# Kernel tuning notes

Hardware: AMD Instinct MI355X
Metric: run time of the kernel (lower is better)

The kernel has to match this reference:

```python
import jax, jax.numpy as jnp
import numpy as np

BOUND = np.array([[-4.0, 4.0], [-4.0, 4.0], [-2.0, 2.0]], dtype=np.float32)
N_PTS = 1048576
PLANE_C = 3
PLANE_RES = [128, 256, 512, 1024]
N_LEVELS = 16
F_PER = 2
T = 2 ** 16  # hashmap size (log2_hashmap_size=16)
BASE_RES = 16
FINEST = int(float((BOUND[:, 1] - BOUND[:, 0]).max()) / 0.02)  # 400
_growth = np.exp(np.log(FINEST / BASE_RES) / (N_LEVELS - 1))
HASH_RES = np.floor(BASE_RES * _growth ** np.arange(N_LEVELS)).astype(np.float32)
PRIMES = jnp.array([1, 2654435761, 805459861], dtype=jnp.uint32)


def setup_inputs() -> dict:
    key = jax.random.key(0)
    ks = jax.random.split(key, 32)
    lo = jnp.asarray(BOUND[:, 0]); hi = jnp.asarray(BOUND[:, 1])
    inp = {}
    inp['p'] = jax.random.uniform(ks[0], (N_PTS, 3), dtype=jnp.float32) * (hi - lo) + lo
    i = 1
    for li, r in enumerate(PLANE_RES):
        for name in ('xy', 'xz', 'yz'):
            inp[f'plane_{name}_{li}'] = 0.1 * jax.random.normal(ks[i], (PLANE_C, r, r), dtype=jnp.float32)
            i += 1
    inp['hash_table'] = jax.random.uniform(ks[i], (N_LEVELS, T, F_PER), dtype=jnp.float32, minval=-1e-4, maxval=1e-4); i += 1

    def lin(k, fi, fo):
        s = 1.0 / np.sqrt(fi)
        k1, k2 = jax.random.split(k)
        return (jax.random.uniform(k1, (fi, fo), minval=-s, maxval=s, dtype=jnp.float32),
                jax.random.uniform(k2, (fo,), minval=-s, maxval=s, dtype=jnp.float32))

    c_in = 12 * PLANE_C + N_LEVELS * F_PER  # 68
    inp['W0'], inp['b0'] = lin(ks[i], c_in, 64); i += 1
    inp['W1'], inp['b1'] = lin(ks[i], 64, 64); i += 1
    inp['Wo'], inp['bo'] = lin(ks[i], 64, 33); i += 1  # 1 sdf + 32 geo_feat
    inp['Wc0'], inp['bc0'] = lin(ks[i], 12 * PLANE_C + 32, 64); i += 1
    inp['Wc1'], inp['bc1'] = lin(ks[i], 64, 32); i += 1
    inp['Wco'], inp['bco'] = lin(ks[i], 32, 3); i += 1
    return inp


def sample_plane(plane, u, v):
    """Bilinear grid_sample, align_corners=True, padding_mode='border'.
    plane: (C,H,W); u indexes W, v indexes H; u,v in [-1,1]. Returns (N,C)."""
    C, H, W = plane.shape
    x = jnp.clip((u + 1.0) * 0.5 * (W - 1), 0.0, W - 1)
    y = jnp.clip((v + 1.0) * 0.5 * (H - 1), 0.0, H - 1)
    x0 = jnp.floor(x); y0 = jnp.floor(y)
    wx = x - x0; wy = y - y0
    x0i = x0.astype(jnp.int32); y0i = y0.astype(jnp.int32)
    x1i = jnp.minimum(x0i + 1, W - 1); y1i = jnp.minimum(y0i + 1, H - 1)
    g = lambda yi, xi: plane[:, yi, xi]  # (C,N)
    out = (g(y0i, x0i) * ((1 - wy) * (1 - wx)) + g(y0i, x1i) * ((1 - wy) * wx)
           + g(y1i, x0i) * (wy * (1 - wx)) + g(y1i, x1i) * (wy * wx))
    return out.T


def hash_encode(p01, table):
    """Multi-res hash grid (instant-ngp style). p01: (N,3) in [0,1]; table: (L,T,F) -> (N, L*F)."""
    res = jnp.asarray(HASH_RES)  # (L,)

    def level(r, tab):
        x = p01 * r
        x0 = jnp.floor(x)
        w = x - x0
        xi = x0.astype(jnp.uint32)  # (N,3)
        feat = jnp.zeros((p01.shape[0], F_PER), dtype=table.dtype)
        for dz in (0, 1):
            for dy in (0, 1):
                for dx in (0, 1):
                    c = xi + jnp.array([dx, dy, dz], dtype=jnp.uint32)
                    h = c * PRIMES[None, :]
                    idx = ((h[:, 0] ^ h[:, 1] ^ h[:, 2]) % T).astype(jnp.int32)
                    wgt = ((w[:, 0] if dx else 1 - w[:, 0])
                           * (w[:, 1] if dy else 1 - w[:, 1])
                           * (w[:, 2] if dz else 1 - w[:, 2]))
                    feat = feat + tab[idx] * wgt[:, None]
        return feat  # (N,F)

    feats = jax.vmap(level, in_axes=(0, 0))(res, table)  # (L,N,F)
    return jnp.transpose(feats, (1, 0, 2)).reshape(p01.shape[0], N_LEVELS * F_PER)


def _forward(p, plane_xy_0, plane_xz_0, plane_yz_0, plane_xy_1, plane_xz_1, plane_yz_1,
             plane_xy_2, plane_xz_2, plane_yz_2, plane_xy_3, plane_xz_3, plane_yz_3,
             hash_table, W0, b0, W1, b1, Wo, bo, Wc0, bc0, Wc1, bc1, Wco, bco):
    bound = jnp.asarray(BOUND)
    p_nor = (p - bound[:, 0]) / (bound[:, 1] - bound[:, 0]) * 2.0 - 1.0  # normalize_3d_coordinate
    u, v, w = p_nor[:, 0], p_nor[:, 1], p_nor[:, 2]
    levels = [(plane_xy_0, plane_xz_0, plane_yz_0), (plane_xy_1, plane_xz_1, plane_yz_1),
              (plane_xy_2, plane_xz_2, plane_yz_2), (plane_xy_3, plane_xz_3, plane_yz_3)]
    feats = []
    for pxy, pxz, pyz in levels:
        feats += [sample_plane(pxy, u, v), sample_plane(pxz, u, w), sample_plane(pyz, v, w)]
    plane_feat = jnp.concatenate(feats, axis=-1)  # (N, 36)
    hfeat = hash_encode((p_nor + 1.0) * 0.5, hash_table)  # (N, 32)
    # SDF branch
    h = jnp.concatenate([plane_feat, hfeat], axis=-1)  # (N, 68)
    h = jax.nn.relu(h @ W0 + b0)
    h = jax.nn.relu(h @ W1 + b1)
    sf = jnp.tanh(h @ Wo + bo)
    sdf, geo_feat = sf[:, :1], sf[:, 1:]
    # RGB branch
    c = jnp.concatenate([geo_feat, plane_feat], axis=-1)  # (N, 68)
    c = jax.nn.relu(c @ Wc0 + bc0)
    c = jax.nn.relu(c @ Wc1 + bc1)
    rgb = jax.nn.sigmoid(c @ Wco + bco)
    return jnp.concatenate([rgb, sdf], axis=-1)  # (N, 4)


def reference(p, plane_xy_0, plane_xz_0, plane_yz_0, plane_xy_1, plane_xz_1, plane_yz_1,
              plane_xy_2, plane_xz_2, plane_yz_2, plane_xy_3, plane_xz_3, plane_yz_3,
              hash_table, W0, b0, W1, b1, Wo, bo, Wc0, bc0, Wc1, bc1, Wco, bco):
    return _forward(p, plane_xy_0, plane_xz_0, plane_yz_0, plane_xy_1, plane_xz_1, plane_yz_1,
                    plane_xy_2, plane_xz_2, plane_yz_2, plane_xy_3, plane_xz_3, plane_yz_3,
                    hash_table, W0, b0, W1, b1, Wo, bo, Wc0, bc0, Wc1, bc1, Wco, bco)
```

## Files before the change

### kernel.cpp

```cpp
#include <hip/hip_runtime.h>

#define NPTS 1048576
#define NBKT 262144

typedef short bhalf8 __attribute__((ext_vector_type(8)));
typedef _Float16 halfv8 __attribute__((ext_vector_type(8)));
typedef _Float16 halfv2 __attribute__((ext_vector_type(2)));
typedef float floatx4 __attribute__((ext_vector_type(4)));

#define WSZ 24320
#define FROWS 21
#define MLP_THREADS 1024
#define MLP_WAVES 16

#define PB_PLANES 16320
#define PB_HASH 4096
#define PB_HIST 4096

__device__ const float HRg[16] = {16.f, 19.f, 24.f, 30.f, 37.f, 46.f, 57.f, 71.f,
                                  89.f, 110.f, 136.f, 169.f, 210.f, 260.f, 322.f, 400.f};


__device__ __forceinline__ float my_tanh(float x) {
  float e = __expf(2.f * x);
  return 1.f - 2.f * __builtin_amdgcn_rcpf(e + 1.f);
}

__device__ __forceinline__ float my_sigmoid(float x) {
  return __builtin_amdgcn_rcpf(1.f + __expf(-x));
}

__device__ __forceinline__ unsigned short f2h(float v) {
  _Float16 h = (_Float16)v;
  unsigned short u;
  __builtin_memcpy(&u, &h, 2);
  return u;
}

__device__ __forceinline__ float h2f(unsigned short u) {
  _Float16 h;
  __builtin_memcpy(&h, &u, 2);
  return (float)h;
}

// ... 19 lines not shown

__device__ __forceinline__ unsigned hash_level(const unsigned* __restrict__ ht, int lv,
                                               float q0, float q1, float q2) {
  const float r = HRg[lv];
  float x0 = q0 * r, x1 = q1 * r, x2 = q2 * r;
  float f0 = floorf(x0), f1 = floorf(x1), f2 = floorf(x2);
  float w0 = x0 - f0, w1 = x1 - f1, w2 = x2 - f2;
  unsigned i0 = (unsigned)(int)f0, i1 = (unsigned)(int)f1, i2 = (unsigned)(int)f2;
  const unsigned* __restrict__ hb = ht + ((unsigned)lv << 16);
  unsigned tv[8];
#pragma unroll
  for (int dz = 0; dz < 2; ++dz)
#pragma unroll
    for (int dy = 0; dy < 2; ++dy)
#pragma unroll
      for (int dx = 0; dx < 2; ++dx) {
        unsigned h = (i0 + dx) ^ ((i1 + dy) * 2654435761u) ^ ((i2 + dz) * 805459861u);
        tv[dz * 4 + dy * 2 + dx] = hb[h & 65535u];
      }
  halfv2 acc2 = {(_Float16)0.f, (_Float16)0.f};
#pragma unroll
  for (int c = 0; c < 8; ++c) {
    const int dx = c & 1, dy = (c >> 1) & 1, dz = c >> 2;
    float wgt = (dx ? w0 : 1.f - w0) * (dy ? w1 : 1.f - w1) * (dz ? w2 : 1.f - w2);
    halfv2 th;
    __builtin_memcpy(&th, &tv[c], 4);
    _Float16 wh = (_Float16)wgt;
    halfv2 w2v = {wh, wh};
    acc2 = th * w2v + acc2;
  }
  unsigned res;
  __builtin_memcpy(&res, &acc2, 4);
  return res;
}


struct PrepParams {
  const float* psrc[12];
  ushort4* pdst[12];
  const float* hash;
  unsigned* hashb;
  const float* p;
  unsigned* hist;
};

__global__ __launch_bounds__(256) void prep_kernel(PrepParams P) {
  const int b = blockIdx.x;
  if (b < PB_PLANES) {
    const int CUM[13] = {0, 16384, 32768, 49152, 114688, 180224, 245760,
                         507904, 770048, 1032192, 2080768, 3129344, 4177920};
    const int RESL[12] = {128, 128, 128, 256, 256, 256, 512, 512, 512, 1024, 1024, 1024};
    const int s = b << 8;
    int pi = 0;
#pragma unroll
    for (int i = 1; i < 12; ++i)
      if (s >= CUM[i]) pi = i;
    const int li = s + threadIdx.x - CUM[pi];
    const int R = RESL[pi];
    const int n = R * R;
    const float* __restrict__ src = P.psrc[pi];
    ushort4 t;
    t.x = f2h(src[li]);
    t.y = f2h(src[n + li]);
    t.z = f2h(src[2 * n + li]);
    t.w = 0;
    P.pdst[pi][li] = t;
  } else if (b < PB_PLANES + PB_HASH) {
    const int i = ((b - PB_PLANES) << 8) + threadIdx.x;
    float2 v = *(const float2*)(P.hash + (size_t)i * 2);
    P.hashb[i] = (unsigned)f2h(v.x) | ((unsigned)f2h(v.y) << 16);
  } else {
    const int i = ((b - PB_PLANES - PB_HASH) << 8) + threadIdx.x;
    const float* pp = P.p + (size_t)i * 3;
    unsigned k = morton_key(pp[0], pp[1], pp[2]);
    atomicAdd(&P.hist[k], 1u);
  }
}


__global__ __launch_bounds__(256) void scan1_kernel(const unsigned* __restrict__ hist,
                                                    unsigned* __restrict__ partial) {
  __shared__ unsigned s[256];
  const int b = blockIdx.x, t = threadIdx.x;
  uint4 v = ((const uint4*)(hist + b * 1024))[t];
  s[t] = v.x + v.y + v.z + v.w;
  __syncthreads();
  for (int d = 128; d > 0; d >>= 1) {
    if (t < d) s[t] += s[t + d];
    __syncthreads();
  }
  if (t == 0) partial[b] = s[0];
}

__global__ __launch_bounds__(256) void scan2_kernel(const unsigned* __restrict__ partial,
                                                    unsigned* __restrict__ base) {
  __shared__ unsigned s[256];
  const int t = threadIdx.x;
  s[t] = partial[t];
  __syncthreads();
  for (int d = 1; d < 256; d <<= 1) {
    unsigned v = (t >= d) ? s[t - d] : 0u;
    __syncthreads();
    s[t] += v;
    __syncthreads();
  }
  base[t] = (t == 0) ? 0u : s[t - 1];
}

__global__ __launch_bounds__(256) void scan3_kernel(const unsigned* __restrict__ hist,
                                                    const unsigned* __restrict__ base,
                                                    unsigned* __restrict__ cursor) {
  __shared__ unsigned s[256];
  const int b = blockIdx.x, t = threadIdx.x;
  uint4 v = ((const uint4*)(hist + b * 1024))[t];
  unsigned sum = v.x + v.y + v.z + v.w;
  s[t] = sum;
  __syncthreads();
  for (int d = 1; d < 256; d <<= 1) {
    unsigned x = (t >= d) ? s[t - d] : 0u;
    __syncthreads();
    s[t] += x;
    __syncthreads();
  }
  unsigned off = base[b] + s[t] - sum;
  uint4 c;
  c.x = off;
  c.y = off + v.x;
  c.z = off + v.x + v.y;
  c.w = off + v.x + v.y + v.z;
  ((uint4*)(cursor + b * 1024))[t] = c;
}

__global__ __launch_bounds__(256) void scatter_kernel(const float* __restrict__ p,
                                                      unsigned* __restrict__ cursor,
                                                      unsigned* __restrict__ perm) {
  int i = blockIdx.x * 256 + threadIdx.x;
  const float* pp = p + (size_t)i * 3;
  unsigned k = morton_key(pp[0], pp[1], pp[2]);
  unsigned slot = atomicAdd(&cursor[k], 1u);
  perm[slot] = (unsigned)i;
}


__global__ __launch_bounds__(256) void repack_plane(const float* __restrict__ src,
                                                    ushort4* __restrict__ dst, int R) {
  int i = blockIdx.x * 256 + threadIdx.x;
  int n = R * R;
  if (i >= n) return;
  ushort4 t;
  t.x = f2h(src[i]);
  t.y = f2h(src[n + i]);
  t.z = f2h(src[2 * n + i]);
  t.w = 0;
  dst[i] = t;
}


__device__ __forceinline__ void sample3i(const uint2* __restrict__ pl,
                                         float a, float b, int R, float* f) {
  const float Rm1 = (float)(R - 1);
  float x = fminf(fmaxf((a + 1.f) * 0.5f * Rm1, 0.f), Rm1);
  float y = fminf(fmaxf((b + 1.f) * 0.5f * Rm1, 0.f), Rm1);
  float x0f = floorf(x), y0f = floorf(y);
  float wx = x - x0f, wy = y - y0f;
  int x0 = (int)x0f, y0 = (int)y0f;
  int x1 = min(x0 + 1, R - 1), y1 = min(y0 + 1, R - 1);
  float w00 = (1.f - wy) * (1.f - wx);
  float w01 = (1.f - wy) * wx;
  float w10 = wy * (1.f - wx);
  float w11 = wy * wx;
  uint2 t00 = pl[y0 * R + x0];
  uint2 t01 = pl[y0 * R + x1];
  uint2 t10 = pl[y1 * R + x0];
  uint2 t11 = pl[y1 * R + x1];
#pragma unroll
  for (int c = 0; c < 3; ++c) {
    f[c] = texch(t00, c) * w00 + texch(t01, c) * w01 +
           texch(t10, c) * w10 + texch(t11, c) * w11;
  }
}

__device__ __forceinline__ void sample3f(const float* __restrict__ pl,
                                         float a, float b, int R, float* f) {
  const float Rm1 = (float)(R - 1);
  float x = fminf(fmaxf((a + 1.f) * 0.5f * Rm1, 0.f), Rm1);
  float y = fminf(fmaxf((b + 1.f) * 0.5f * Rm1, 0.f), Rm1);
  float x0f = floorf(x), y0f = floorf(y);
  float wx = x - x0f, wy = y - y0f;
  int x0 = (int)x0f, y0 = (int)y0f;
  int x1 = min(x0 + 1, R - 1), y1 = min(y0 + 1, R - 1);
  float w00 = (1.f - wy) * (1.f - wx);
  float w01 = (1.f - wy) * wx;
  float w10 = wy * (1.f - wx);
  float w11 = wy * wx;
  int i00 = y0 * R + x0, i01 = y0 * R + x1;
  int i10 = y1 * R + x0, i11 = y1 * R + x1;
  const int R2 = R * R;
#pragma unroll
  for (int c = 0; c < 3; ++c) {
    const float* base = pl + c * R2;
    f[c] = base[i00] * w00 + base[i01] * w01 + base[i10] * w10 + base[i11] * w11;
  }
}


struct FeatParams {
  const float* p;
  const uint2* pli[12];
  const unsigned* perm;
  unsigned* fbuf;
};

template <bool SORT>
__global__ __launch_bounds__(256) void feat_kernel(FeatParams P) {
  int bid = blockIdx.x;
  if (SORT) bid = (bid & 7) * (NPTS / 256 / 8) + (bid >> 3);
  const int tid = bid * 256 + threadIdx.x;
  const int pid = SORT ? (int)P.perm[tid] : tid;

  const float* __restrict__ pp = P.p + (size_t)pid * 3;
  const float px = pp[0], py = pp[1], pz = pp[2];

  const float u = (px + 4.f) * 0.25f - 1.f;
  const float v = (py + 4.f) * 0.25f - 1.f;
  const float w = (pz + 2.f) * 0.5f - 1.f;

  float pf[36];
  {
    const int RES[4] = {128, 256, 512, 1024};
#pragma unroll
    for (int li = 0; li < 4; ++li) {
      sample3i(P.pli[li * 3 + 0], u, v, RES[li], &pf[li * 9 + 0]);
      sample3i(P.pli[li * 3 + 1], u, w, RES[li], &pf[li * 9 + 3]);
      sample3i(P.pli[li * 3 + 2], v, w, RES[li], &pf[li * 9 + 6]);
    }
  }
  unsigned* __restrict__ F = P.fbuf;
#pragma unroll
  for (int kk = 0; kk < 18; ++kk) {
    unsigned pk = (unsigned)f2h(pf[2 * kk]) | ((unsigned)f2h(pf[2 * kk + 1]) << 16);
    F[(size_t)kk * NPTS + tid] = pk;
  }
  F[(size_t)18 * NPTS + tid] = __float_as_uint((px + 4.f) * 0.125f);
  F[(size_t)19 * NPTS + tid] = __float_as_uint((py + 4.f) * 0.125f);
  F[(size_t)20 * NPTS + tid] = __float_as_uint((pz + 2.f) * 0.25f);
}


struct MlpWParams {
  const unsigned* fbuf;
  const unsigned* perm;
  const unsigned* hashb;
  const float* W0; const float* b0;
  const float* W1; const float* b1;
  const float* Wo; const float* bo;
  const float* Wc0; const float* bc0;
  const float* Wc1; const float* bc1;
  const float* Wco; const float* bco;
  float* out;
};

__device__ __forceinline__ void stage_w(const float* __restrict__ src, int K, int Nsrc,
                                        int STR, int NPAD, int OFF, short* Wlds, int tid) {
  const int total = NPAD * STR;
  for (int idx = tid; idx < total; idx += MLP_THREADS) {
    int c = idx / STR;
    int k = idx - c * STR;
    float val = (k < K && c < Nsrc) ? src[k * Nsrc + c] : 0.f;
    Wlds[OFF + idx] = (short)f2h(val);
  }
}

__device__ __forceinline__ void stage_b(const float* __restrict__ src, int Nsrc, int NPAD,
                                        int BOFF, float* Blds, int tid) {
  for (int j = tid; j < NPAD; j += MLP_THREADS) Blds[BOFF + j] = (j < Nsrc) ? src[j] : 0.f;
}

__device__ __forceinline__ halfv8 as_h8(bhalf8 s) {
  halfv8 h;
  __builtin_memcpy(&h, &s, 16);
  return h;
}

__device__ __forceinline__ halfv8 ldA(const unsigned* __restrict__ fbuf, int pt,
                                      int kkBase, int kkLim) {
  bhalf8 r;
#pragma unroll
  for (int j = 0; j < 4; ++j) {
    const int kk = kkBase + j;
    unsigned d = 0u;
    if (kk < kkLim) d = fbuf[(size_t)kk * NPTS + pt];
    r[2 * j] = (short)(d & 0xffffu);
    r[2 * j + 1] = (short)(d >> 16);
  }
  return as_h8(r);
}

__device__ __forceinline__ halfv8 frag4(unsigned d0, unsigned d1, unsigned d2, unsigned d3) {
  bhalf8 r;
  r[0] = (short)(d0 & 0xffffu); r[1] = (short)(d0 >> 16);
  r[2] = (short)(d1 & 0xffffu); r[3] = (short)(d1 >> 16);
  r[4] = (short)(d2 & 0xffffu); r[5] = (short)(d2 >> 16);
  r[6] = (short)(d3 & 0xffffu); r[7] = (short)(d3 >> 16);
  return as_h8(r);
}

__device__ __forceinline__ halfv8 ldS(const short* scr, int rowl, int grp, int s) {
  return *(const halfv8*)&scr[rowl * 72 + 32 * s + 8 * grp];
}

template <int NT, int KS, int OFF, int STR>
__device__ __forceinline__ void mlayer(const halfv8 (&af)[KS], floatx4 (&acc)[NT],
                                       const short* Wlds, int rowl, int grp) {
#pragma unroll
  for (int n = 0; n < NT; ++n) {
    floatx4 a{};
#pragma unroll
    for (int s = 0; s < KS; ++s) {
      const int wo = OFF + (16 * n + rowl) * STR + 32 * s + 8 * grp;
      const halfv8 wA = *(const halfv8*)&Wlds[wo];
      a = __builtin_amdgcn_mfma_f32_16x16x32_f16(wA, af[s], a, 0, 0, 0);
    }
    acc[n] = a;
  }
}

template <int NT>
__device__ __forceinline__ void relu_wr(const floatx4 (&acc)[NT], const float* Blds,
                                        int boff, short* scr, int rowl, int grp) {
#pragma unroll
  for (int n = 0; n < NT; ++n) {
    const int cbase = 16 * n + 4 * grp;
    short4 v4;
    float v0 = fmaxf(acc[n][0] + Blds[boff + cbase + 0], 0.f);
    float v1 = fmaxf(acc[n][1] + Blds[boff + cbase + 1], 0.f);
    float v2 = fmaxf(acc[n][2] + Blds[boff + cbase + 2], 0.f);
    float v3 = fmaxf(acc[n][3] + Blds[boff + cbase + 3], 0.f);
    v4.x = (short)f2h(v0);
    v4.y = (short)f2h(v1);
    v4.z = (short)f2h(v2);
    v4.w = (short)f2h(v3);
    *(short4*)&scr[rowl * 72 + cbase] = v4;
  }
}

__device__ __forceinline__ void tanh_wr(const floatx4 (&acc)[3], const float* Blds,
                                        short* scr, float* ost, int rowl, int grp) {
#pragma unroll
  for (int n = 0; n < 3; ++n) {
#pragma unroll
    for (int r = 0; r < 4; ++r) {
      const int c = 16 * n + 4 * grp + r;
      float v = my_tanh(acc[n][r] + Blds[128 + c]);
      if (c == 0) ost[rowl * 4 + 3] = v;
      if (c >= 1 && c <= 32) scr[rowl * 72 + c - 1] = (short)f2h(v);
    }
  }
}

template <bool SORT>
__global__ __launch_bounds__(MLP_THREADS) void mlp_mfma(MlpWParams P) {
  __shared__ short Wlds[WSZ];
  __shared__ float Blds[288];
  __shared__ short Scr[MLP_WAVES * 16 * 72];
  __shared__ float Ost[MLP_WAVES][16][4];

  const int tid = threadIdx.x;

  stage_w(P.W0,  68, 64, 104, 64,     0, Wlds, tid);
  stage_w(P.W1,  64, 64,  72, 64,  6656, Wlds, tid);
  stage_w(P.Wo,  64, 33,  72, 48, 11264, Wlds, tid);
  stage_w(P.Wc0, 68, 64, 104, 64, 14720, Wlds, tid);
  stage_w(P.Wc1, 64, 32,  72, 32, 21376, Wlds, tid);
  stage_w(P.Wco, 32,  3,  40, 16, 23680, Wlds, tid);
  stage_b(P.b0,  64, 64,   0, Blds, tid);
  stage_b(P.b1,  64, 64,  64, Blds, tid);
  stage_b(P.bo,  33, 48, 128, Blds, tid);
  stage_b(P.bc0, 64, 64, 176, Blds, tid);
  stage_b(P.bc1, 32, 32, 240, Blds, tid);
  stage_b(P.bco,  3, 16, 272, Blds, tid);
  __syncthreads();

  const int wave = tid >> 6, lane = tid & 63;
  const int rowl = lane & 15, grp = lane >> 4;
  short* scr0 = &Scr[wave * 16 * 72];
  float* ost0 = &Ost[wave][0][0];

  const int lv0 = (grp == 0) ? 0 : (4 * grp - 2);

  for (int t = 0; t < 8; ++t) {
    const int wbase = ((blockIdx.x * 8 + t) * MLP_WAVES + wave) * 16;
    const int ptA = wbase + rowl;

    halfv8 af0A;
    unsigned pA16, pA17;

    {
      const unsigned* __restrict__ F = P.fbuf;
      float qA0 = __uint_as_float(F[(size_t)18 * NPTS + ptA]);
      float qA1 = __uint_as_float(F[(size_t)19 * NPTS + ptA]);
      float qA2 = __uint_as_float(F[(size_t)20 * NPTS + ptA]);

      unsigned hA0, hA1, hA2, hA3;
      {
        const int l0 = lv0, l1 = lv0 + 1;
        const int l2 = (grp == 0) ? 14 : (lv0 + 2);
        const int l3 = (grp == 0) ? 15 : (lv0 + 3);
        hA0 = hash_level(P.hashb, l0, qA0, qA1, qA2);
        hA1 = hash_level(P.hashb, l1, qA0, qA1, qA2);
        hA2 = hash_level(P.hashb, l2, qA0, qA1, qA2);
        hA3 = hash_level(P.hashb, l3, qA0, qA1, qA2);
      }

      pA16 = F[(size_t)16 * NPTS + ptA];
      pA17 = F[(size_t)17 * NPTS + ptA];

      halfv8 s1A = (grp == 0) ? frag4(pA16, pA17, hA0, hA1) : frag4(hA0, hA1, hA2, hA3);
      halfv8 s2A = (grp == 0) ? frag4(hA2, hA3, 0u, 0u) : frag4(0u, 0u, 0u, 0u);

      af0A = ldA(P.fbuf, ptA, 4 * grp, 18);
      halfv8 afA[3] = {af0A, s1A, s2A};
      floatx4 accA[4];
      mlayer<4, 3, 0, 104>(afA, accA, Wlds, rowl, grp);
      relu_wr<4>(accA, Blds, 0, scr0, rowl, grp);
    }
    {
      halfv8 afA[2] = {ldS(scr0, rowl, grp, 0), ldS(scr0, rowl, grp, 1)};
      floatx4 accA[4];
      mlayer<4, 2, 6656, 72>(afA, accA, Wlds, rowl, grp);
      relu_wr<4>(accA, Blds, 64, scr0, rowl, grp);
    }
    {
      halfv8 afA[2] = {ldS(scr0, rowl, grp, 0), ldS(scr0, rowl, grp, 1)};
      floatx4 accA[3];
      mlayer<3, 2, 11264, 72>(afA, accA, Wlds, rowl, grp);
      tanh_wr(accA, Blds, scr0, ost0, rowl, grp);
    }
    {
      halfv8 s2 = (grp == 0) ? frag4(pA16, pA17, 0u, 0u) : frag4(0u, 0u, 0u, 0u);
      halfv8 afA[3] = {ldS(scr0, rowl, grp, 0), af0A, s2};
      floatx4 accA[4];
      mlayer<4, 3, 14720, 104>(afA, accA, Wlds, rowl, grp);
      relu_wr<4>(accA, Blds, 176, scr0, rowl, grp);
    }
    {
      halfv8 afA[2] = {ldS(scr0, rowl, grp, 0), ldS(scr0, rowl, grp, 1)};
      floatx4 accA[2];
      mlayer<2, 2, 21376, 72>(afA, accA, Wlds, rowl, grp);
      relu_wr<2>(accA, Blds, 240, scr0, rowl, grp);
    }
    {
      halfv8 afA[1] = {ldS(scr0, rowl, grp, 0)};
      floatx4 accA[1];
      mlayer<1, 1, 23680, 40>(afA, accA, Wlds, rowl, grp);
#pragma unroll
      for (int r = 0; r < 4; ++r) {
        const int c = 4 * grp + r;
        if (c < 3) {
          float vA = my_sigmoid(accA[0][r] + Blds[272 + c]);
          ost0[rowl * 4 + c] = vA;
        }
      }
    }

    if (lane < 16) {
      float4 o = *(float4*)&Ost[wave][lane][0];
      int dst = SORT ? (int)P.perm[wbase + lane] : (wbase + lane);
      ((float4*)P.out)[dst] = o;
    }
  }
}


struct DecParams {
  const float* p;
  const float* pl[12];
  const uint2* pli[12];
  const float* hash;
  const float* W0; const float* b0;
  const float* W1; const float* b1;
  const float* Wo; const float* bo;
  const float* Wc0; const float* bc0;
  const float* Wc1; const float* bc1;
  const float* Wco; const float* bco;
  float* out;
};

template <bool ILV>
__global__ __launch_bounds__(256) void dec_kernel(DecParams P) {
  const int tid = blockIdx.x * 256 + threadIdx.x;

  const float* __restrict__ pp = P.p + (size_t)tid * 3;
  const float px = pp[0], py = pp[1], pz = pp[2];

  const float u = (px + 4.f) * 0.25f - 1.f;
  const float v = (py + 4.f) * 0.25f - 1.f;
  const float w = (pz + 2.f) * 0.5f - 1.f;

  float feat[68];
  {
    const int RES[4] = {128, 256, 512, 1024};
// ... 105 lines not shown
  float c1[32];
#pragma unroll
  for (int j = 0; j < 32; ++j) c1[j] = P.bc1[j];
#pragma unroll
  for (int i = 0; i < 64; ++i) {
    const float a = hid[i];
    const float* wr = P.Wc1 + i * 32;
#pragma unroll
    for (int j = 0; j < 32; ++j) c1[j] = fmaf(a, wr[j], c1[j]);
  }

  float r0 = P.bco[0], r1 = P.bco[1], r2 = P.bco[2];
#pragma unroll
  for (int i = 0; i < 32; ++i) {
    const float a = fmaxf(c1[i], 0.f);
    r0 = fmaf(a, P.Wco[i * 3 + 0], r0);
    r1 = fmaf(a, P.Wco[i * 3 + 1], r1);
    r2 = fmaf(a, P.Wco[i * 3 + 2], r2);
  }

  float4 o;
  o.x = my_sigmoid(r0);
  o.y = my_sigmoid(r1);
  o.z = my_sigmoid(r2);
  o.w = sdf;
  ((float4*)P.out)[tid] = o;
}


extern "C" void kernel_launch(void* const* d_in, const int* in_sizes, int n_in,
                              void* d_out, int out_size, void* d_ws, size_t ws_size,
                              hipStream_t stream) {
  const int RES[4] = {128, 256, 512, 1024};
  const size_t planes_bytes = (size_t)3 * (128 * 128 + 256 * 256 + 512 * 512 + 1024 * 1024) * 8;
  const size_t hash_bytes = (size_t)16 * 65536 * 4;
  const size_t feat_bytes = (size_t)FROWS * NPTS * 4;
  const size_t perm_bytes = (size_t)NPTS * 4;
  const size_t hist_bytes = (size_t)NBKT * 4;
  const size_t need_full = planes_bytes + hash_bytes + feat_bytes + 64;
  const size_t need_sort = need_full + perm_bytes + 2 * hist_bytes + 4096;
  const size_t need_mid = planes_bytes + 64;

  char* wsp = (char*)d_ws;
  const float* p = (const float*)d_in[0];

  if (ws_size >= need_sort) {
    size_t off = 0;
    PrepParams PP;
    PP.p = p;
    PP.hash = (const float*)d_in[13];
    const uint2* pli[12];
    for (int i = 0; i < 12; ++i) {
      int R = RES[i / 3];
      PP.psrc[i] = (const float*)d_in[1 + i];
      PP.pdst[i] = (ushort4*)(wsp + off);
      pli[i] = (const uint2*)(wsp + off);
      off += (size_t)R * R * 8;
    }
    unsigned* hashb = (unsigned*)(wsp + off);
    PP.hashb = hashb;
    off += hash_bytes;
    unsigned* fbuf = (unsigned*)(wsp + off);
    off += feat_bytes;
    unsigned* perm = (unsigned*)(wsp + off);
    off += perm_bytes;
    unsigned* hist = (unsigned*)(wsp + off);
    off += hist_bytes;
    unsigned* cursor = (unsigned*)(wsp + off);
    off += hist_bytes;
    unsigned* partial = (unsigned*)(wsp + off);
    off += 1024;
    unsigned* base = (unsigned*)(wsp + off);
    off += 1024;
    PP.hist = hist;

    hipMemsetAsync(hist, 0, hist_bytes, stream);
    prep_kernel<<<PB_PLANES + PB_HASH + PB_HIST, 256, 0, stream>>>(PP);
    scan1_kernel<<<256, 256, 0, stream>>>(hist, partial);
    scan2_kernel<<<1, 256, 0, stream>>>(partial, base);
    scan3_kernel<<<256, 256, 0, stream>>>(hist, base, cursor);
    scatter_kernel<<<NPTS / 256, 256, 0, stream>>>(p, cursor, perm);

    FeatParams FP;
    FP.p = p;
    for (int i = 0; i < 12; ++i) FP.pli[i] = pli[i];
    FP.perm = perm;
    FP.fbuf = fbuf;
    feat_kernel<true><<<NPTS / 256, 256, 0, stream>>>(FP);

    MlpWParams MP;
    MP.fbuf = fbuf;
    MP.perm = perm;
    MP.hashb = hashb;
    MP.W0 = (const float*)d_in[14]; MP.b0 = (const float*)d_in[15];
    MP.W1 = (const float*)d_in[16]; MP.b1 = (const float*)d_in[17];
    MP.Wo = (const float*)d_in[18]; MP.bo = (const float*)d_in[19];
    MP.Wc0 = (const float*)d_in[20]; MP.bc0 = (const float*)d_in[21];
    MP.Wc1 = (const float*)d_in[22]; MP.bc1 = (const float*)d_in[23];
    MP.Wco = (const float*)d_in[24]; MP.bco = (const float*)d_in[25];
    MP.out = (float*)d_out;
    mlp_mfma<true><<<512, MLP_THREADS, 0, stream>>>(MP);
    return;
  }

  if (ws_size >= need_full) {
    size_t off = 0;
    PrepParams PP;
    PP.p = p;
    PP.hash = (const float*)d_in[13];
    const uint2* pli[12];
    for (int i = 0; i < 12; ++i) {
      int R = RES[i / 3];
      PP.psrc[i] = (const float*)d_in[1 + i];
      PP.pdst[i] = (ushort4*)(wsp + off);
      pli[i] = (const uint2*)(wsp + off);
      off += (size_t)R * R * 8;
    }
    unsigned* hashb = (unsigned*)(wsp + off);
    PP.hashb = hashb;
    off += hash_bytes;
    unsigned* fbuf = (unsigned*)(wsp + off);
    PP.hist = nullptr;

    prep_kernel<<<PB_PLANES + PB_HASH, 256, 0, stream>>>(PP);

    FeatParams FP;
    FP.p = p;
    for (int i = 0; i < 12; ++i) FP.pli[i] = pli[i];
    FP.perm = nullptr;
    FP.fbuf = fbuf;
    feat_kernel<false><<<NPTS / 256, 256, 0, stream>>>(FP);

    MlpWParams MP;
    MP.fbuf = fbuf;
    MP.perm = nullptr;
    MP.hashb = hashb;
    MP.W0 = (const float*)d_in[14]; MP.b0 = (const float*)d_in[15];
    MP.W1 = (const float*)d_in[16]; MP.b1 = (const float*)d_in[17];
    MP.Wo = (const float*)d_in[18]; MP.bo = (const float*)d_in[19];
    MP.Wc0 = (const float*)d_in[20]; MP.bc0 = (const float*)d_in[21];
    MP.Wc1 = (const float*)d_in[22]; MP.bc1 = (const float*)d_in[23];
    MP.Wco = (const float*)d_in[24]; MP.bco = (const float*)d_in[25];
    MP.out = (float*)d_out;
    mlp_mfma<false><<<512, MLP_THREADS, 0, stream>>>(MP);
    return;
  }

  DecParams P;
  P.p = p;
  for (int i = 0; i < 12; ++i) P.pl[i] = (const float*)d_in[1 + i];
  P.hash = (const float*)d_in[13];
  P.W0  = (const float*)d_in[14]; P.b0  = (const float*)d_in[15];
  P.W1  = (const float*)d_in[16]; P.b1  = (const float*)d_in[17];
  P.Wo  = (const float*)d_in[18]; P.bo  = (const float*)d_in[19];
  P.Wc0 = (const float*)d_in[20]; P.bc0 = (const float*)d_in[21];
  P.Wc1 = (const float*)d_in[22]; P.bc1 = (const float*)d_in[23];
  P.Wco = (const float*)d_in[24]; P.bco = (const float*)d_in[25];
  P.out = (float*)d_out;

  if (ws_size >= need_mid) {
    size_t off = 0;
    for (int i = 0; i < 12; ++i) {
      int R = RES[i / 3];
      int n = R * R;
      P.pli[i] = (const uint2*)(wsp + off);
      repack_plane<<<(n + 255) / 256, 256, 0, stream>>>(
          (const float*)d_in[1 + i], (ushort4*)(wsp + off), R);
      off += (size_t)n * 8;
    }
    dec_kernel<true><<<NPTS / 256, 256, 0, stream>>>(P);
  } else {
    for (int i = 0; i < 12; ++i) P.pli[i] = nullptr;
    dec_kernel<false><<<NPTS / 256, 256, 0, stream>>>(P);
  }
}
```

Before: 388.8 us.

## Fuse plane sampling into MLP kernel and scatter sorted coords directly

Drops the separate feature kernel and its 21-row intermediate buffer. Plane bilinear sampling now runs inside the MLP kernel on packed fp16 planes, with each lane group sampling planes that match its MFMA K-slice, and the W0/Wc0 staging is remapped to the new padded 4-channel layout. The scatter kernel writes sorted normalized coordinates plus the original index as a float4, which replaces the perm indirection. This removes a large global write/read round trip, at the cost of more gather latency and register pressure inside the MLP kernel, and the non-sort fallback path is removed.

```diff
diff --git a/kernel.cpp b/kernel.cpp
--- a/kernel.cpp
+++ b/kernel.cpp
@@ -9,7 +9,6 @@
 typedef float floatx4 __attribute__((ext_vector_type(4)));
 
 #define WSZ 24320
-#define FROWS 21
 #define MLP_THREADS 1024
 #define MLP_WAVES 16
 
@@ -95,6 +94,43 @@
   unsigned res;
   __builtin_memcpy(&res, &acc2, 4);
   return res;
+}
+
+__device__ __forceinline__ uint2 sampleP(const uint2* __restrict__ planes, int s,
+                                         float u, float v, float w) {
+  const int level = s / 3;
+  const int m = s - level * 3;
+  const float a = (m == 2) ? v : u;
+  const float b = (m == 0) ? v : w;
+  const int R = 128 << level;
+  const unsigned base = 16384u * ((1u << (2 * level)) - 1u) + (unsigned)m * (unsigned)(R * R);
+  const float Rm1 = (float)(R - 1);
+  float x = fminf(fmaxf((a + 1.f) * 0.5f * Rm1, 0.f), Rm1);
+  float y = fminf(fmaxf((b + 1.f) * 0.5f * Rm1, 0.f), Rm1);
+  float x0f = floorf(x), y0f = floorf(y);
+  float wx = x - x0f, wy = y - y0f;
+  int x0 = (int)x0f, y0 = (int)y0f;
+  int x1 = min(x0 + 1, R - 1), y1 = min(y0 + 1, R - 1);
+  uint2 t00 = planes[base + y0 * R + x0];
+  uint2 t01 = planes[base + y0 * R + x1];
+  uint2 t10 = planes[base + y1 * R + x0];
+  uint2 t11 = planes[base + y1 * R + x1];
+  _Float16 h00 = (_Float16)((1.f - wy) * (1.f - wx));
+  _Float16 h01 = (_Float16)((1.f - wy) * wx);
+  _Float16 h10 = (_Float16)(wy * (1.f - wx));
+  _Float16 h11 = (_Float16)(wy * wx);
+  halfv2 w00 = {h00, h00}, w01 = {h01, h01}, w10 = {h10, h10}, w11 = {h11, h11};
+  halfv2 l00, l01, l10, l11, u00, u01, u10, u11;
+  __builtin_memcpy(&l00, &t00.x, 4); __builtin_memcpy(&u00, &t00.y, 4);
+  __builtin_memcpy(&l01, &t01.x, 4); __builtin_memcpy(&u01, &t01.y, 4);
+  __builtin_memcpy(&l10, &t10.x, 4); __builtin_memcpy(&u10, &t10.y, 4);
+  __builtin_memcpy(&l11, &t11.x, 4); __builtin_memcpy(&u11, &t11.y, 4);
+  halfv2 alo = l00 * w00 + l01 * w01 + l10 * w10 + l11 * w11;
+  halfv2 ahi = u00 * w00 + u01 * w01 + u10 * w10 + u11 * w11;
+  uint2 r;
+  __builtin_memcpy(&r.x, &alo, 4);
+  __builtin_memcpy(&r.y, &ahi, 4);
+  return r;
 }
 
 
@@ -196,12 +232,18 @@
 
 __global__ __launch_bounds__(256) void scatter_kernel(const float* __restrict__ p,
                                                       unsigned* __restrict__ cursor,
-                                                      unsigned* __restrict__ perm) {
+                                                      float4* __restrict__ qs) {
   int i = blockIdx.x * 256 + threadIdx.x;
   const float* pp = p + (size_t)i * 3;
-  unsigned k = morton_key(pp[0], pp[1], pp[2]);
+  const float px = pp[0], py = pp[1], pz = pp[2];
+  unsigned k = morton_key(px, py, pz);
   unsigned slot = atomicAdd(&cursor[k], 1u);
-  perm[slot] = (unsigned)i;
+  float4 q;
+  q.x = (px + 4.f) * 0.125f;
+  q.y = (py + 4.f) * 0.125f;
+  q.z = (pz + 2.f) * 0.25f;
+  q.w = __uint_as_float((unsigned)i);
+  qs[slot] = q;
 }
 
 
@@ -267,53 +309,10 @@
 }
 
 
-struct FeatParams {
-  const float* p;
-  const uint2* pli[12];
-  const unsigned* perm;
-  unsigned* fbuf;
-};
-
-template <bool SORT>
-__global__ __launch_bounds__(256) void feat_kernel(FeatParams P) {
-  int bid = blockIdx.x;
-  if (SORT) bid = (bid & 7) * (NPTS / 256 / 8) + (bid >> 3);
-  const int tid = bid * 256 + threadIdx.x;
-  const int pid = SORT ? (int)P.perm[tid] : tid;
-
-  const float* __restrict__ pp = P.p + (size_t)pid * 3;
-  const float px = pp[0], py = pp[1], pz = pp[2];
-
-  const float u = (px + 4.f) * 0.25f - 1.f;
-  const float v = (py + 4.f) * 0.25f - 1.f;
-  const float w = (pz + 2.f) * 0.5f - 1.f;
-
-  float pf[36];
-  {
-    const int RES[4] = {128, 256, 512, 1024};
-#pragma unroll
-    for (int li = 0; li < 4; ++li) {
-      sample3i(P.pli[li * 3 + 0], u, v, RES[li], &pf[li * 9 + 0]);
-      sample3i(P.pli[li * 3 + 1], u, w, RES[li], &pf[li * 9 + 3]);
-      sample3i(P.pli[li * 3 + 2], v, w, RES[li], &pf[li * 9 + 6]);
-    }
-  }
-  unsigned* __restrict__ F = P.fbuf;
-#pragma unroll
-  for (int kk = 0; kk < 18; ++kk) {
-    unsigned pk = (unsigned)f2h(pf[2 * kk]) | ((unsigned)f2h(pf[2 * kk + 1]) << 16);
-    F[(size_t)kk * NPTS + tid] = pk;
-  }
-  F[(size_t)18 * NPTS + tid] = __float_as_uint((px + 4.f) * 0.125f);
-  F[(size_t)19 * NPTS + tid] = __float_as_uint((py + 4.f) * 0.125f);
-  F[(size_t)20 * NPTS + tid] = __float_as_uint((pz + 2.f) * 0.25f);
-}
-
-
 struct MlpWParams {
-  const unsigned* fbuf;
-  const unsigned* perm;
+  const uint2* planes;
   const unsigned* hashb;
+  const float4* qs;
   const float* W0; const float* b0;
   const float* W1; const float* b1;
   const float* Wo; const float* bo;
@@ -323,13 +322,32 @@
   float* out;
 };
 
+template <int MODE>
 __device__ __forceinline__ void stage_w(const float* __restrict__ src, int K, int Nsrc,
                                         int STR, int NPAD, int OFF, short* Wlds, int tid) {
   const int total = NPAD * STR;
   for (int idx = tid; idx < total; idx += MLP_THREADS) {
     int c = idx / STR;
-    int k = idx - c * STR;
-    float val = (k < K && c < Nsrc) ? src[k * Nsrc + c] : 0.f;
+    int kp = idx - c * STR;
+    int sk = -1;
+    if (MODE == 0) {
+      if (kp < 48) {
+        int s = kp >> 2, ch = kp & 3;
+        if (ch < 3) sk = s * 3 + ch;
+      } else if (kp < 80) {
+        sk = 36 + (kp - 48);
+      }
+    } else if (MODE == 1) {
+      if (kp < 32) {
+        sk = kp;
+      } else if (kp < 80) {
+        int s = (kp - 32) >> 2, ch = (kp - 32) & 3;
+        if (ch < 3) sk = 32 + s * 3 + ch;
+      }
+    } else {
+      if (kp < K) sk = kp;
+    }
+    float val = (sk >= 0 && c < Nsrc) ? src[sk * Nsrc + c] : 0.f;
     Wlds[OFF + idx] = (short)f2h(val);
   }
 }
@@ -343,20 +361,6 @@
   halfv8 h;
   __builtin_memcpy(&h, &s, 16);
   return h;
-}
-
-__device__ __forceinline__ halfv8 ldA(const unsigned* __restrict__ fbuf, int pt,
-                                      int kkBase, int kkLim) {
-  bhalf8 r;
-#pragma unroll
-  for (int j = 0; j < 4; ++j) {
-    const int kk = kkBase + j;
-    unsigned d = 0u;
-    if (kk < kkLim) d = fbuf[(size_t)kk * NPTS + pt];
-    r[2 * j] = (short)(d & 0xffffu);
-    r[2 * j + 1] = (short)(d >> 16);
-  }
-  return as_h8(r);
 }
 
 __device__ __forceinline__ halfv8 frag4(unsigned d0, unsigned d1, unsigned d2, unsigned d3) {
@@ -421,8 +425,7 @@
   }
 }
 
-template <bool SORT>
-__global__ __launch_bounds__(MLP_THREADS) void mlp_mfma(MlpWParams P) {
+__global__ __launch_bounds__(MLP_THREADS) void mlp_fused(MlpWParams P) {
   __shared__ short Wlds[WSZ];
   __shared__ float Blds[288];
   __shared__ short Scr[MLP_WAVES * 16 * 72];
@@ -430,12 +433,12 @@
 
   const int tid = threadIdx.x;
 
-  stage_w(P.W0,  68, 64, 104, 64,     0, Wlds, tid);
-  stage_w(P.W1,  64, 64,  72, 64,  6656, Wlds, tid);
-  stage_w(P.Wo,  64, 33,  72, 48, 11264, Wlds, tid);
-  stage_w(P.Wc0, 68, 64, 104, 64, 14720, Wlds, tid);
-  stage_w(P.Wc1, 64, 32,  72, 32, 21376, Wlds, tid);
-  stage_w(P.Wco, 32,  3,  40, 16, 23680, Wlds, tid);
+  stage_w<0>(P.W0,  96, 64, 104, 64,     0, Wlds, tid);
+  stage_w<2>(P.W1,  64, 64,  72, 64,  6656, Wlds, tid);
+  stage_w<2>(P.Wo,  64, 33,  72, 48, 11264, Wlds, tid);
+  stage_w<1>(P.Wc0, 96, 64, 104, 64, 14720, Wlds, tid);
+  stage_w<2>(P.Wc1, 64, 32,  72, 32, 21376, Wlds, tid);
+  stage_w<2>(P.Wco, 32,  3,  40, 16, 23680, Wlds, tid);
   stage_b(P.b0,  64, 64,   0, Blds, tid);
   stage_b(P.b1,  64, 64,  64, Blds, tid);
   stage_b(P.bo,  33, 48, 128, Blds, tid);
@@ -449,40 +452,40 @@
   short* scr0 = &Scr[wave * 16 * 72];
   float* ost0 = &Ost[wave][0][0];
 
-  const int lv0 = (grp == 0) ? 0 : (4 * grp - 2);
+  int bid = blockIdx.x;
+  bid = (bid & 7) * 64 + (bid >> 3);
 
   for (int t = 0; t < 8; ++t) {
-    const int wbase = ((blockIdx.x * 8 + t) * MLP_WAVES + wave) * 16;
-    const int ptA = wbase + rowl;
-
-    halfv8 af0A;
-    unsigned pA16, pA17;
+    const int wbase = ((bid * 8 + t) * MLP_WAVES + wave) * 16;
+    const int pt = wbase + rowl;
+
+    float4 q4 = P.qs[pt];
+    const float q0 = q4.x, q1 = q4.y, q2 = q4.z;
+    const unsigned pid = __float_as_uint(q4.w);
+    const float u = 2.f * q0 - 1.f;
+    const float v = 2.f * q1 - 1.f;
+    const float w = 2.f * q2 - 1.f;
+
+    uint2 sA = sampleP(P.planes, 2 * grp, u, v, w);
+    uint2 sB = sampleP(P.planes, 2 * grp + 1, u, v, w);
+    uint2 sC = {0u, 0u}, sD = {0u, 0u};
+    if (grp < 2) {
+      sC = sampleP(P.planes, 8 + 2 * grp, u, v, w);
+      sD = sampleP(P.planes, 9 + 2 * grp, u, v, w);
+    }
+    const int lbase = (grp < 2) ? (8 + 4 * grp) : (4 * grp - 8);
+    unsigned h0 = hash_level(P.hashb, lbase + 0, q0, q1, q2);
+    unsigned h1 = hash_level(P.hashb, lbase + 1, q0, q1, q2);
+    unsigned h2 = hash_level(P.hashb, lbase + 2, q0, q1, q2);
+    unsigned h3 = hash_level(P.hashb, lbase + 3, q0, q1, q2);
+
+    halfv8 af0 = frag4(sA.x, sA.y, sB.x, sB.y);
+    halfv8 af1 = (grp < 2) ? frag4(sC.x, sC.y, sD.x, sD.y) : frag4(h0, h1, h2, h3);
+    halfv8 af2 = (grp < 2) ? frag4(h0, h1, h2, h3) : frag4(0u, 0u, 0u, 0u);
+    halfv8 zf = frag4(0u, 0u, 0u, 0u);
 
     {
-      const unsigned* __restrict__ F = P.fbuf;
-      float qA0 = __uint_as_float(F[(size_t)18 * NPTS + ptA]);
-      float qA1 = __uint_as_float(F[(size_t)19 * NPTS + ptA]);
-      float qA2 = __uint_as_float(F[(size_t)20 * NPTS + ptA]);
-
-      unsigned hA0, hA1, hA2, hA3;
-      {
-        const int l0 = lv0, l1 = lv0 + 1;
-        const int l2 = (grp == 0) ? 14 : (lv0 + 2);
-        const int l3 = (grp == 0) ? 15 : (lv0 + 3);
-        hA0 = hash_level(P.hashb, l0, qA0, qA1, qA2);
-        hA1 = hash_level(P.hashb, l1, qA0, qA1, qA2);
-        hA2 = hash_level(P.hashb, l2, qA0, qA1, qA2);
-        hA3 = hash_level(P.hashb, l3, qA0, qA1, qA2);
-      }
-
-      pA16 = F[(size_t)16 * NPTS + ptA];
-      pA17 = F[(size_t)17 * NPTS + ptA];
-
-      halfv8 s1A = (grp == 0) ? frag4(pA16, pA17, hA0, hA1) : frag4(hA0, hA1, hA2, hA3);
-      halfv8 s2A = (grp == 0) ? frag4(hA2, hA3, 0u, 0u) : frag4(0u, 0u, 0u, 0u);
-
-      af0A = ldA(P.fbuf, ptA, 4 * grp, 18);
-      halfv8 afA[3] = {af0A, s1A, s2A};
+      halfv8 afA[3] = {af0, af1, af2};
       floatx4 accA[4];
       mlayer<4, 3, 0, 104>(afA, accA, Wlds, rowl, grp);
       relu_wr<4>(accA, Blds, 0, scr0, rowl, grp);
@@ -500,8 +503,7 @@
       tanh_wr(accA, Blds, scr0, ost0, rowl, grp);
     }
     {
-      halfv8 s2 = (grp == 0) ? frag4(pA16, pA17, 0u, 0u) : frag4(0u, 0u, 0u, 0u);
-      halfv8 afA[3] = {ldS(scr0, rowl, grp, 0), af0A, s2};
+      halfv8 afA[3] = {ldS(scr0, rowl, grp, 0), af0, (grp < 2) ? af1 : zf};
       floatx4 accA[4];
       mlayer<4, 3, 14720, 104>(afA, accA, Wlds, rowl, grp);
       relu_wr<4>(accA, Blds, 176, scr0, rowl, grp);
@@ -528,8 +530,7 @@
 
     if (lane < 16) {
       float4 o = *(float4*)&Ost[wave][lane][0];
-      int dst = SORT ? (int)P.perm[wbase + lane] : (wbase + lane);
-      ((float4*)P.out)[dst] = o;
+      ((float4*)P.out)[pid] = o;
     }
   }
 }
@@ -701,38 +702,33 @@
                               void* d_out, int out_size, void* d_ws, size_t ws_size,
                               hipStream_t stream) {
   const int RES[4] = {128, 256, 512, 1024};
-  const size_t planes_bytes = (size_t)3 * (128 * 128 + 256 * 256 + 512 * 512 + 1024 * 1024) * 8;
+  const size_t planes_bytes = (size_t)4177920 * 8;
   const size_t hash_bytes = (size_t)16 * 65536 * 4;
-  const size_t feat_bytes = (size_t)FROWS * NPTS * 4;
-  const size_t perm_bytes = (size_t)NPTS * 4;
+  const size_t qs_bytes = (size_t)NPTS * 16;
   const size_t hist_bytes = (size_t)NBKT * 4;
-  const size_t need_full = planes_bytes + hash_bytes + feat_bytes + 64;
-  const size_t need_sort = need_full + perm_bytes + 2 * hist_bytes + 4096;
+  const size_t need_fused = planes_bytes + hash_bytes + qs_bytes + 2 * hist_bytes + 4096;
   const size_t need_mid = planes_bytes + 64;
 
   char* wsp = (char*)d_ws;
   const float* p = (const float*)d_in[0];
 
-  if (ws_size >= need_sort) {
+  if (ws_size >= need_fused) {
     size_t off = 0;
     PrepParams PP;
     PP.p = p;
     PP.hash = (const float*)d_in[13];
-    const uint2* pli[12];
+    const uint2* planes = (const uint2*)wsp;
     for (int i = 0; i < 12; ++i) {
       int R = RES[i / 3];
       PP.psrc[i] = (const float*)d_in[1 + i];
       PP.pdst[i] = (ushort4*)(wsp + off);
-      pli[i] = (const uint2*)(wsp + off);
       off += (size_t)R * R * 8;
     }
     unsigned* hashb = (unsigned*)(wsp + off);
     PP.hashb = hashb;
     off += hash_bytes;
-    unsigned* fbuf = (unsigned*)(wsp + off);
-    off += feat_bytes;
-    unsigned* perm = (unsigned*)(wsp + off);
-    off += perm_bytes;
+    float4* qs = (float4*)(wsp + off);
+    off += qs_bytes;
     unsigned* hist = (unsigned*)(wsp + off);
     off += hist_bytes;
     unsigned* cursor = (unsigned*)(wsp + off);
@@ -748,19 +744,12 @@
     scan1_kernel<<<256, 256, 0, stream>>>(hist, partial);
     scan2_kernel<<<1, 256, 0, stream>>>(partial, base);
     scan3_kernel<<<256, 256, 0, stream>>>(hist, base, cursor);
-    scatter_kernel<<<NPTS / 256, 256, 0, stream>>>(p, cursor, perm);
-
-    FeatParams FP;
-    FP.p = p;
-    for (int i = 0; i < 12; ++i) FP.pli[i] = pli[i];
-    FP.perm = perm;
-    FP.fbuf = fbuf;
-    feat_kernel<true><<<NPTS / 256, 256, 0, stream>>>(FP);
+    scatter_kernel<<<NPTS / 256, 256, 0, stream>>>(p, cursor, qs);
 
     MlpWParams MP;
-    MP.fbuf = fbuf;
-    MP.perm = perm;
+    MP.planes = planes;
     MP.hashb = hashb;
+    MP.qs = qs;
     MP.W0 = (const float*)d_in[14]; MP.b0 = (const float*)d_in[15];
     MP.W1 = (const float*)d_in[16]; MP.b1 = (const float*)d_in[17];
     MP.Wo = (const float*)d_in[18]; MP.bo = (const float*)d_in[19];
@@ -768,50 +757,7 @@
     MP.Wc1 = (const float*)d_in[22]; MP.bc1 = (const float*)d_in[23];
     MP.Wco = (const float*)d_in[24]; MP.bco = (const float*)d_in[25];
     MP.out = (float*)d_out;
-    mlp_mfma<true><<<512, MLP_THREADS, 0, stream>>>(MP);
-    return;
-  }
-
-  if (ws_size >= need_full) {
-    size_t off = 0;
-    PrepParams PP;
-    PP.p = p;
-    PP.hash = (const float*)d_in[13];
-    const uint2* pli[12];
-    for (int i = 0; i < 12; ++i) {
-      int R = RES[i / 3];
-      PP.psrc[i] = (const float*)d_in[1 + i];
-      PP.pdst[i] = (ushort4*)(wsp + off);
-      pli[i] = (const uint2*)(wsp + off);
-      off += (size_t)R * R * 8;
-    }
-    unsigned* hashb = (unsigned*)(wsp + off);
-    PP.hashb = hashb;
-    off += hash_bytes;
-    unsigned* fbuf = (unsigned*)(wsp + off);
-    PP.hist = nullptr;
-
-    prep_kernel<<<PB_PLANES + PB_HASH, 256, 0, stream>>>(PP);
-
-    FeatParams FP;
-    FP.p = p;
-    for (int i = 0; i < 12; ++i) FP.pli[i] = pli[i];
-    FP.perm = nullptr;
-    FP.fbuf = fbuf;
-    feat_kernel<false><<<NPTS / 256, 256, 0, stream>>>(FP);
-
-    MlpWParams MP;
-    MP.fbuf = fbuf;
-    MP.perm = nullptr;
-    MP.hashb = hashb;
-    MP.W0 = (const float*)d_in[14]; MP.b0 = (const float*)d_in[15];
-    MP.W1 = (const float*)d_in[16]; MP.b1 = (const float*)d_in[17];
-    MP.Wo = (const float*)d_in[18]; MP.bo = (const float*)d_in[19];
-    MP.Wc0 = (const float*)d_in[20]; MP.bc0 = (const float*)d_in[21];
-    MP.Wc1 = (const float*)d_in[22]; MP.bc1 = (const float*)d_in[23];
-    MP.Wco = (const float*)d_in[24]; MP.bco = (const float*)d_in[25];
-    MP.out = (float*)d_out;
-    mlp_mfma<false><<<512, MLP_THREADS, 0, stream>>>(MP);
+    mlp_fused<<<512, MLP_THREADS, 0, stream>>>(MP);
     return;
   }
 
```

Result: slower. 418.8 us (+7.7%).

## Scatter normalized coordinates directly into sorted order and merge scan kernels

Applied to the files above, without the earlier changes.

The scatter kernel now writes each point's normalized coordinates and original index as a float4 into sorted slots, replacing the permutation array. The feature kernel therefore reads contiguous float4s instead of gathering through perm into p. The original index is carried as an extra feature row so the MLP can write outputs directly. The second and third scan kernels are merged into one, removing a launch and the base buffer. The MLP block order is also swizzled, and the unsorted fallback path is removed, so the kernel now needs the larger sort workspace.

```diff
diff --git a/kernel.cpp b/kernel.cpp
--- a/kernel.cpp
+++ b/kernel.cpp
@@ -9,7 +9,7 @@
 typedef float floatx4 __attribute__((ext_vector_type(4)));
 
 #define WSZ 24320
-#define FROWS 21
+#define FROWS 22
 #define MLP_THREADS 1024
 #define MLP_WAVES 16
 
@@ -155,37 +155,33 @@
   if (t == 0) partial[b] = s[0];
 }
 
-__global__ __launch_bounds__(256) void scan2_kernel(const unsigned* __restrict__ partial,
-                                                    unsigned* __restrict__ base) {
-  __shared__ unsigned s[256];
-  const int t = threadIdx.x;
-  s[t] = partial[t];
+__global__ __launch_bounds__(256) void scan23_kernel(const unsigned* __restrict__ hist,
+                                                     const unsigned* __restrict__ partial,
+                                                     unsigned* __restrict__ cursor) {
+  __shared__ unsigned sp[256];
+  __shared__ unsigned s2[256];
+  const int b = blockIdx.x, t = threadIdx.x;
+  sp[t] = partial[t];
   __syncthreads();
   for (int d = 1; d < 256; d <<= 1) {
-    unsigned v = (t >= d) ? s[t - d] : 0u;
+    unsigned v = (t >= d) ? sp[t - d] : 0u;
     __syncthreads();
-    s[t] += v;
+    sp[t] += v;
     __syncthreads();
   }
-  base[t] = (t == 0) ? 0u : s[t - 1];
-}
-
-__global__ __launch_bounds__(256) void scan3_kernel(const unsigned* __restrict__ hist,
-                                                    const unsigned* __restrict__ base,
-                                                    unsigned* __restrict__ cursor) {
-  __shared__ unsigned s[256];
-  const int b = blockIdx.x, t = threadIdx.x;
+  const unsigned base = (b == 0) ? 0u : sp[b - 1];
+
   uint4 v = ((const uint4*)(hist + b * 1024))[t];
   unsigned sum = v.x + v.y + v.z + v.w;
-  s[t] = sum;
+  s2[t] = sum;
   __syncthreads();
   for (int d = 1; d < 256; d <<= 1) {
-    unsigned x = (t >= d) ? s[t - d] : 0u;
+    unsigned x = (t >= d) ? s2[t - d] : 0u;
     __syncthreads();
-    s[t] += x;
+    s2[t] += x;
     __syncthreads();
   }
-  unsigned off = base[b] + s[t] - sum;
+  unsigned off = base + s2[t] - sum;
   uint4 c;
   c.x = off;
   c.y = off + v.x;
@@ -196,12 +192,18 @@
 
 __global__ __launch_bounds__(256) void scatter_kernel(const float* __restrict__ p,
                                                       unsigned* __restrict__ cursor,
-                                                      unsigned* __restrict__ perm) {
+                                                      float4* __restrict__ qs) {
   int i = blockIdx.x * 256 + threadIdx.x;
   const float* pp = p + (size_t)i * 3;
-  unsigned k = morton_key(pp[0], pp[1], pp[2]);
+  const float px = pp[0], py = pp[1], pz = pp[2];
+  unsigned k = morton_key(px, py, pz);
   unsigned slot = atomicAdd(&cursor[k], 1u);
-  perm[slot] = (unsigned)i;
+  float4 q;
+  q.x = (px + 4.f) * 0.125f;
+  q.y = (py + 4.f) * 0.125f;
+  q.z = (pz + 2.f) * 0.25f;
+  q.w = __uint_as_float((unsigned)i);
+  qs[slot] = q;
 }
 
 
@@ -268,25 +270,20 @@
 
 
 struct FeatParams {
-  const float* p;
+  const float4* qs;
   const uint2* pli[12];
-  const unsigned* perm;
   unsigned* fbuf;
 };
 
-template <bool SORT>
 __global__ __launch_bounds__(256) void feat_kernel(FeatParams P) {
   int bid = blockIdx.x;
-  if (SORT) bid = (bid & 7) * (NPTS / 256 / 8) + (bid >> 3);
+  bid = (bid & 7) * (NPTS / 256 / 8) + (bid >> 3);
   const int tid = bid * 256 + threadIdx.x;
-  const int pid = SORT ? (int)P.perm[tid] : tid;
-
-  const float* __restrict__ pp = P.p + (size_t)pid * 3;
-  const float px = pp[0], py = pp[1], pz = pp[2];
-
-  const float u = (px + 4.f) * 0.25f - 1.f;
-  const float v = (py + 4.f) * 0.25f - 1.f;
-  const float w = (pz + 2.f) * 0.5f - 1.f;
+
+  float4 q4 = P.qs[tid];
+  const float u = 2.f * q4.x - 1.f;
+  const float v = 2.f * q4.y - 1.f;
+  const float w = 2.f * q4.z - 1.f;
 
   float pf[36];
   {
@@ -304,15 +301,15 @@
     unsigned pk = (unsigned)f2h(pf[2 * kk]) | ((unsigned)f2h(pf[2 * kk + 1]) << 16);
     F[(size_t)kk * NPTS + tid] = pk;
   }
-  F[(size_t)18 * NPTS + tid] = __float_as_uint((px + 4.f) * 0.125f);
-  F[(size_t)19 * NPTS + tid] = __float_as_uint((py + 4.f) * 0.125f);
-  F[(size_t)20 * NPTS + tid] = __float_as_uint((pz + 2.f) * 0.25f);
+  F[(size_t)18 * NPTS + tid] = __float_as_uint(q4.x);
+  F[(size_t)19 * NPTS + tid] = __float_as_uint(q4.y);
+  F[(size_t)20 * NPTS + tid] = __float_as_uint(q4.z);
+  F[(size_t)21 * NPTS + tid] = __float_as_uint(q4.w);
 }
 
 
 struct MlpWParams {
   const unsigned* fbuf;
-  const unsigned* perm;
   const unsigned* hashb;
   const float* W0; const float* b0;
   const float* W1; const float* b1;
@@ -421,7 +418,6 @@
   }
 }
 
-template <bool SORT>
 __global__ __launch_bounds__(MLP_THREADS) void mlp_mfma(MlpWParams P) {
   __shared__ short Wlds[WSZ];
   __shared__ float Blds[288];
@@ -451,18 +447,23 @@
 
   const int lv0 = (grp == 0) ? 0 : (4 * grp - 2);
 
+  int bid = blockIdx.x;
+  bid = (bid & 7) * 64 + (bid >> 3);
+
   for (int t = 0; t < 8; ++t) {
-    const int wbase = ((blockIdx.x * 8 + t) * MLP_WAVES + wave) * 16;
+    const int wbase = ((bid * 8 + t) * MLP_WAVES + wave) * 16;
     const int ptA = wbase + rowl;
 
     halfv8 af0A;
     unsigned pA16, pA17;
+    unsigned pid;
 
     {
       const unsigned* __restrict__ F = P.fbuf;
       float qA0 = __uint_as_float(F[(size_t)18 * NPTS + ptA]);
       float qA1 = __uint_as_float(F[(size_t)19 * NPTS + ptA]);
       float qA2 = __uint_as_float(F[(size_t)20 * NPTS + ptA]);
+      pid = F[(size_t)21 * NPTS + ptA];
 
       unsigned hA0, hA1, hA2, hA3;
       {
@@ -528,8 +529,7 @@
 
     if (lane < 16) {
       float4 o = *(float4*)&Ost[wave][lane][0];
-      int dst = SORT ? (int)P.perm[wbase + lane] : (wbase + lane);
-      ((float4*)P.out)[dst] = o;
+      ((float4*)P.out)[pid] = o;
     }
   }
 }
@@ -701,13 +701,13 @@
                               void* d_out, int out_size, void* d_ws, size_t ws_size,
                               hipStream_t stream) {
   const int RES[4] = {128, 256, 512, 1024};
-  const size_t planes_bytes = (size_t)3 * (128 * 128 + 256 * 256 + 512 * 512 + 1024 * 1024) * 8;
+  const size_t planes_bytes = (size_t)4177920 * 8;
   const size_t hash_bytes = (size_t)16 * 65536 * 4;
   const size_t feat_bytes = (size_t)FROWS * NPTS * 4;
-  const size_t perm_bytes = (size_t)NPTS * 4;
+  const size_t qs_bytes = (size_t)NPTS * 16;
   const size_t hist_bytes = (size_t)NBKT * 4;
-  const size_t need_full = planes_bytes + hash_bytes + feat_bytes + 64;
-  const size_t need_sort = need_full + perm_bytes + 2 * hist_bytes + 4096;
+  const size_t need_sort = planes_bytes + hash_bytes + feat_bytes + qs_bytes +
+                           2 * hist_bytes + 4096;
   const size_t need_mid = planes_bytes + 64;
 
   char* wsp = (char*)d_ws;
@@ -731,35 +731,30 @@
     off += hash_bytes;
     unsigned* fbuf = (unsigned*)(wsp + off);
     off += feat_bytes;
-    unsigned* perm = (unsigned*)(wsp + off);
-    off += perm_bytes;
+    float4* qs = (float4*)(wsp + off);
+    off += qs_bytes;
     unsigned* hist = (unsigned*)(wsp + off);
     off += hist_bytes;
     unsigned* cursor = (unsigned*)(wsp + off);
     off += hist_bytes;
     unsigned* partial = (unsigned*)(wsp + off);
-    off += 1024;
-    unsigned* base = (unsigned*)(wsp + off);
-    off += 1024;
+    off += 2048;
     PP.hist = hist;
 
     hipMemsetAsync(hist, 0, hist_bytes, stream);
     prep_kernel<<<PB_PLANES + PB_HASH + PB_HIST, 256, 0, stream>>>(PP);
     scan1_kernel<<<256, 256, 0, stream>>>(hist, partial);
-    scan2_kernel<<<1, 256, 0, stream>>>(partial, base);
-    scan3_kernel<<<256, 256, 0, stream>>>(hist, base, cursor);
-    scatter_kernel<<<NPTS / 256, 256, 0, stream>>>(p, cursor, perm);
+    scan23_kernel<<<256, 256, 0, stream>>>(hist, partial, cursor);
+    scatter_kernel<<<NPTS / 256, 256, 0, stream>>>(p, cursor, qs);
 
     FeatParams FP;
-    FP.p = p;
+    FP.qs = qs;
     for (int i = 0; i < 12; ++i) FP.pli[i] = pli[i];
-    FP.perm = perm;
     FP.fbuf = fbuf;
-    feat_kernel<true><<<NPTS / 256, 256, 0, stream>>>(FP);
+    feat_kernel<<<NPTS / 256, 256, 0, stream>>>(FP);
 
     MlpWParams MP;
     MP.fbuf = fbuf;
-    MP.perm = perm;
     MP.hashb = hashb;
     MP.W0 = (const float*)d_in[14]; MP.b0 = (const float*)d_in[15];
     MP.W1 = (const float*)d_in[16]; MP.b1 = (const float*)d_in[17];
@@ -768,50 +763,7 @@
     MP.Wc1 = (const float*)d_in[22]; MP.bc1 = (const float*)d_in[23];
     MP.Wco = (const float*)d_in[24]; MP.bco = (const float*)d_in[25];
     MP.out = (float*)d_out;
-    mlp_mfma<true><<<512, MLP_THREADS, 0, stream>>>(MP);
-    return;
-  }
-
-  if (ws_size >= need_full) {
-    size_t off = 0;
-    PrepParams PP;
-    PP.p = p;
-    PP.hash = (const float*)d_in[13];
-    const uint2* pli[12];
-    for (int i = 0; i < 12; ++i) {
-      int R = RES[i / 3];
-      PP.psrc[i] = (const float*)d_in[1 + i];
-      PP.pdst[i] = (ushort4*)(wsp + off);
-      pli[i] = (const uint2*)(wsp + off);
-      off += (size_t)R * R * 8;
-    }
-    unsigned* hashb = (unsigned*)(wsp + off);
-    PP.hashb = hashb;
-    off += hash_bytes;
-    unsigned* fbuf = (unsigned*)(wsp + off);
-    PP.hist = nullptr;
-
-    prep_kernel<<<PB_PLANES + PB_HASH, 256, 0, stream>>>(PP);
-
-    FeatParams FP;
-    FP.p = p;
-    for (int i = 0; i < 12; ++i) FP.pli[i] = pli[i];
-    FP.perm = nullptr;
-    FP.fbuf = fbuf;
-    feat_kernel<false><<<NPTS / 256, 256, 0, stream>>>(FP);
-
-    MlpWParams MP;
-    MP.fbuf = fbuf;
-    MP.perm = nullptr;
-    MP.hashb = hashb;
-    MP.W0 = (const float*)d_in[14]; MP.b0 = (const float*)d_in[15];
-    MP.W1 = (const float*)d_in[16]; MP.b1 = (const float*)d_in[17];
-    MP.Wo = (const float*)d_in[18]; MP.bo = (const float*)d_in[19];
-    MP.Wc0 = (const float*)d_in[20]; MP.bc0 = (const float*)d_in[21];
-    MP.Wc1 = (const float*)d_in[22]; MP.bc1 = (const float*)d_in[23];
-    MP.Wco = (const float*)d_in[24]; MP.bco = (const float*)d_in[25];
-    MP.out = (float*)d_out;
-    mlp_mfma<false><<<512, MLP_THREADS, 0, stream>>>(MP);
+    mlp_mfma<<<512, MLP_THREADS, 0, stream>>>(MP);
     return;
   }
 
```

Result: faster. 377.4 us (median of 2 runs) (-2.9%).
